# Optimization experiments

Hardware: AMD Instinct MI355X
Metric: run time of the kernel (lower is better)

Reference implementation:

```python
import jax, jax.numpy as jnp
import numpy as np

L, B, H = 2048, 128, 300

def setup_inputs() -> dict:
    key = jax.random.key(0)
    k1, k2, k3, k4 = jax.random.split(key, 4)
    hidden = jax.random.normal(k1, (H, B), dtype=jnp.float32)
    question_vector = jax.random.normal(k2, (L, B, H), dtype=jnp.float32)
    W = jax.random.normal(k3, (H, H), dtype=jnp.float32) * (1.0 / np.sqrt(H))
    b = jax.random.normal(k4, (H,), dtype=jnp.float32) * 0.01
    return {"hidden": hidden, "question_vector": question_vector, "W": W, "b": b}

def reference(hidden, question_vector, W, b):
    # nn.Linear: q @ W^T + b, applied per (l, b) token -> [L, B, H]
    proj = jnp.einsum('lbh,kh->lbk', question_vector, W) + b
    # energies[b, l] = hidden[:, b] . proj[l, b]  -> [B, L]
    energies = jnp.einsum('lbh,hb->bl', proj, hidden)
    attn = jax.nn.softmax(energies, axis=-1)
    return attn[None, :, :]  # [1, B, L]
```

## Files before the change

### kernel.cpp

```cpp
#include <hip/hip_runtime.h>
#include <math.h>

#define LL 2048
#define BB 128
#define HH 300
#define HV4 75

__global__ void __launch_bounds__(256) compute_v(const float* __restrict__ W,
                                                 const float* __restrict__ hidden,
                                                 float* __restrict__ v_t) {
    int t = blockIdx.x * blockDim.x + threadIdx.x;
    if (t >= BB * HH) return;
    int b = t / HH;
    int h = t - b * HH;
    float s = 0.f;
#pragma unroll 4
    for (int k = 0; k < HH; ++k)
        s = fmaf(W[k * HH + h], hidden[k * BB + b], s);
    v_t[b * HH + h] = s;
}

__global__ void __launch_bounds__(256) compute_energies(
        const float4* __restrict__ qv4,
        const float4* __restrict__ v4,
        float* __restrict__ energies) {
    int wave = threadIdx.x >> 6;
    int lane = threadIdx.x & 63;
    int row  = blockIdx.x * 4 + wave;
    int b    = row & (BB - 1);

    const float4* q = qv4 + (size_t)row * HV4;
    const float4* v = v4  + (size_t)b   * HV4;

    float4 a0 = q[lane];
    float4 b0 = v[lane];
    float s = a0.x * b0.x + a0.y * b0.y + a0.z * b0.z + a0.w * b0.w;
    if (lane < HV4 - 64) {
        float4 a1 = q[64 + lane];
        float4 b1 = v[64 + lane];
        s += a1.x * b1.x + a1.y * b1.y + a1.z * b1.z + a1.w * b1.w;
    }
#pragma unroll
    for (int off = 32; off > 0; off >>= 1)
        s += __shfl_down(s, off, 64);
    if (lane == 0)
        energies[row] = s;
}

__global__ void __launch_bounds__(256) softmax_rows(
        const float* __restrict__ energies,
        float* __restrict__ out) {
    int b    = blockIdx.x;
    int tid  = threadIdx.x;
    int lane = tid & 63;
    int wave = tid >> 6;

    __shared__ float redm[4];
    __shared__ float reds[4];

    float vals[8];
    float m = -INFINITY;
#pragma unroll
    for (int i = 0; i < 8; ++i) {
        int l = tid + i * 256;
        vals[i] = energies[l * BB + b];
        m = fmaxf(m, vals[i]);
    }
#pragma unroll
    for (int off = 32; off > 0; off >>= 1)
        m = fmaxf(m, __shfl_down(m, off, 64));
    if (lane == 0) redm[wave] = m;
    __syncthreads();
    m = fmaxf(fmaxf(redm[0], redm[1]), fmaxf(redm[2], redm[3]));

    float s = 0.f;
#pragma unroll
    for (int i = 0; i < 8; ++i) {
        vals[i] = __expf(vals[i] - m);
        s += vals[i];
    }
#pragma unroll
    for (int off = 32; off > 0; off >>= 1)
        s += __shfl_down(s, off, 64);
    if (lane == 0) reds[wave] = s;
    __syncthreads();
    s = reds[0] + reds[1] + reds[2] + reds[3];
    float inv = 1.f / s;

#pragma unroll
    for (int i = 0; i < 8; ++i)
        out[b * LL + tid + i * 256] = vals[i] * inv;
}

extern "C" void kernel_launch(void* const* d_in, const int* in_sizes, int n_in,
                              void* d_out, int out_size, void* d_ws, size_t ws_size,
                              hipStream_t stream) {
    const float* hidden = (const float*)d_in[0];
    const float* qv     = (const float*)d_in[1];
    const float* W      = (const float*)d_in[2];
    float* out = (float*)d_out;

    float* v_t      = (float*)d_ws;
    float* energies = v_t + BB * HH;

    compute_v<<<(BB * HH + 255) / 256, 256, 0, stream>>>(W, hidden, v_t);
    compute_energies<<<(LL * BB) / 4, 256, 0, stream>>>(
        (const float4*)qv, (const float4*)v_t, energies);
    softmax_rows<<<BB, 256, 0, stream>>>(energies, out);
}
```

Before: 449.8 us.

## Reorder energy computation to batch-major and vectorize softmax reads/writes

Energies are now written in [B][L] layout by mapping waves with batch as the major index, so the softmax kernel can use contiguous float4 loads and stores instead of strided gathers. compute_v launches one block per batch column and stages the hidden column in shared memory. The energy kernel's wave ordering changes the access order over the large question tensor, which may affect DRAM locality. compute_v now uses fewer blocks, reducing parallelism.

```diff
diff --git a/kernel.cpp b/kernel.cpp
--- a/kernel.cpp
+++ b/kernel.cpp
@@ -9,28 +9,31 @@
 __global__ void __launch_bounds__(256) compute_v(const float* __restrict__ W,
                                                  const float* __restrict__ hidden,
                                                  float* __restrict__ v_t) {
-    int t = blockIdx.x * blockDim.x + threadIdx.x;
-    if (t >= BB * HH) return;
-    int b = t / HH;
-    int h = t - b * HH;
-    float s = 0.f;
+    int b   = blockIdx.x;
+    int tid = threadIdx.x;
+    __shared__ float hcol[HH];
+    for (int k = tid; k < HH; k += 256) hcol[k] = hidden[k * BB + b];
+    __syncthreads();
+    for (int h = tid; h < HH; h += 256) {
+        float s = 0.f;
 #pragma unroll 4
-    for (int k = 0; k < HH; ++k)
-        s = fmaf(W[k * HH + h], hidden[k * BB + b], s);
-    v_t[b * HH + h] = s;
+        for (int k = 0; k < HH; ++k)
+            s = fmaf(W[k * HH + h], hcol[k], s);
+        v_t[b * HH + h] = s;
+    }
 }
 
 __global__ void __launch_bounds__(256) compute_energies(
         const float4* __restrict__ qv4,
         const float4* __restrict__ v4,
         float* __restrict__ energies) {
-    int wave = threadIdx.x >> 6;
+    int w    = blockIdx.x * 4 + (threadIdx.x >> 6);
     int lane = threadIdx.x & 63;
-    int row  = blockIdx.x * 4 + wave;
-    int b    = row & (BB - 1);
+    int b    = w >> 11;
+    int l    = w & (LL - 1);
 
-    const float4* q = qv4 + (size_t)row * HV4;
-    const float4* v = v4  + (size_t)b   * HV4;
+    const float4* q = qv4 + (size_t)(l * BB + b) * HV4;
+    const float4* v = v4  + (size_t)b * HV4;
 
     float4 a0 = q[lane];
     float4 b0 = v[lane];
@@ -44,7 +47,7 @@
     for (int off = 32; off > 0; off >>= 1)
         s += __shfl_down(s, off, 64);
     if (lane == 0)
-        energies[row] = s;
+        energies[b * LL + l] = s;
 }
 
 __global__ void __launch_bounds__(256) softmax_rows(
@@ -58,14 +61,12 @@
     __shared__ float redm[4];
     __shared__ float reds[4];
 
-    float vals[8];
-    float m = -INFINITY;
-#pragma unroll
-    for (int i = 0; i < 8; ++i) {
-        int l = tid + i * 256;
-        vals[i] = energies[l * BB + b];
-        m = fmaxf(m, vals[i]);
-    }
+    const float4* e4 = (const float4*)(energies + (size_t)b * LL);
+    float4 x0 = e4[tid];
+    float4 x1 = e4[tid + 256];
+
+    float m = fmaxf(fmaxf(fmaxf(x0.x, x0.y), fmaxf(x0.z, x0.w)),
+                    fmaxf(fmaxf(x1.x, x1.y), fmaxf(x1.z, x1.w)));
 #pragma unroll
     for (int off = 32; off > 0; off >>= 1)
         m = fmaxf(m, __shfl_down(m, off, 64));
@@ -73,12 +74,11 @@
     __syncthreads();
     m = fmaxf(fmaxf(redm[0], redm[1]), fmaxf(redm[2], redm[3]));
 
-    float s = 0.f;
-#pragma unroll
-    for (int i = 0; i < 8; ++i) {
-        vals[i] = __expf(vals[i] - m);
-        s += vals[i];
-    }
+    x0.x = __expf(x0.x - m); x0.y = __expf(x0.y - m);
+    x0.z = __expf(x0.z - m); x0.w = __expf(x0.w - m);
+    x1.x = __expf(x1.x - m); x1.y = __expf(x1.y - m);
+    x1.z = __expf(x1.z - m); x1.w = __expf(x1.w - m);
+    float s = (x0.x + x0.y + x0.z + x0.w) + (x1.x + x1.y + x1.z + x1.w);
 #pragma unroll
     for (int off = 32; off > 0; off >>= 1)
         s += __shfl_down(s, off, 64);
@@ -87,9 +87,12 @@
     s = reds[0] + reds[1] + reds[2] + reds[3];
     float inv = 1.f / s;
 
-#pragma unroll
-    for (int i = 0; i < 8; ++i)
-        out[b * LL + tid + i * 256] = vals[i] * inv;
+    x0.x *= inv; x0.y *= inv; x0.z *= inv; x0.w *= inv;
+    x1.x *= inv; x1.y *= inv; x1.z *= inv; x1.w *= inv;
+
+    float4* o4 = (float4*)(out + (size_t)b * LL);
+    o4[tid]       = x0;
+    o4[tid + 256] = x1;
 }
 
 extern "C" void kernel_launch(void* const* d_in, const int* in_sizes, int n_in,
@@ -103,7 +106,7 @@
     float* v_t      = (float*)d_ws;
     float* energies = v_t + BB * HH;
 
-    compute_v<<<(BB * HH + 255) / 256, 256, 0, stream>>>(W, hidden, v_t);
+    compute_v<<<BB, 256, 0, stream>>>(W, hidden, v_t);
     compute_energies<<<(LL * BB) / 4, 256, 0, stream>>>(
         (const float4*)qv, (const float4*)v_t, energies);
     softmax_rows<<<BB, 256, 0, stream>>>(energies, out);
```

After: 491.2 us. 9.2% more time.
